# Optimization experiments

Measured on AMD Instinct MI355X. Metric: run time of the kernel, lower is better.

Reference implementation:

```python
import jax, jax.numpy as jnp
import numpy as np

NPAT, NCON, E, H, L = 50000, 20000, 800000, 128, 2
DP, DC = 64, 128
N = NPAT + NCON  # homogeneous node count


def setup_inputs() -> dict:
    key = jax.random.key(0)
    k = jax.random.split(key, 12)
    s = 0.05
    return {
        "x_patient": jax.random.normal(k[0], (NPAT, DP), jnp.float32),
        "x_concept": jax.random.normal(k[1], (NCON, DC), jnp.float32),
        "W_p": jax.random.normal(k[2], (DP, H), jnp.float32) * s,
        "b_p": jnp.zeros((H,), jnp.float32),
        "W_c": jax.random.normal(k[3], (DC, H), jnp.float32) * s,
        "b_c": jnp.zeros((H,), jnp.float32),
        "W_root": jax.random.normal(k[4], (L, H, H), jnp.float32) * s,
        "b_root": jnp.zeros((L, H), jnp.float32),
        "W_rel": jax.random.normal(k[5], (L, 2, H, H), jnp.float32) * s,
        "src_pc": jax.random.randint(k[6], (E,), 0, NPAT),
        "dst_pc": jax.random.randint(k[7], (E,), 0, NCON),
        "src_cp": jax.random.randint(k[8], (E,), 0, NCON),
        "dst_cp": jax.random.randint(k[9], (E,), 0, NPAT),
    }


def reference(x_patient, x_concept, W_p, b_p, W_c, b_c, W_root, b_root, W_rel,
              src_pc, dst_pc, src_cp, dst_cp):
    # per-node-type linear projection, then concat into homogeneous graph
    # (patient offset 0, concept offset NPAT)
    x = jnp.concatenate([x_patient @ W_p + b_p, x_concept @ W_c + b_c], axis=0)  # [N, H]
    rel_edges = [(src_pc, dst_pc + NPAT), (src_cp + NPAT, dst_cp)]
    ones = jnp.ones((E,), jnp.float32)
    # per-relation in-degree for mean aggregation (zero-deg nodes -> 0 output)
    counts = [jnp.maximum(jax.ops.segment_sum(ones, d, num_segments=N), 1.0)[:, None]
              for _, d in rel_edges]
    for l in range(L):
        out = x @ W_root[l] + b_root[l]  # root transform + bias
        for r, (src, dst) in enumerate(rel_edges):
            msg = x[src] @ W_rel[l, r]  # [E, H] gather + relation transform
            out = out + jax.ops.segment_sum(msg, dst, num_segments=N) / counts[r]
        x = jax.nn.relu(out)
    return x  # [N, H]; rows [0:NPAT] are patient embeddings, rest concepts
```

## Files before the change

kernel.cpp:

```cpp
#include <hip/hip_runtime.h>
#include <hip/hip_bf16.h>

#define NPAT 50000
#define NCON 20000
#define NN   70000
#define EE   800000
#define H    128

#define NCON_AL  20032
#define SEGN     (NCON_AL + NPAT)
#define NBUCK    1095
#define RELSPLIT_B 313
#define BUCKCAP  5120
#define SUBS     16
#define SUBCAP   (BUCKCAP / SUBS)
#define BPE      4096
#define NBB      ((2 * EE + BPE - 1) / BPE)
#define CAP      4096

typedef __attribute__((ext_vector_type(8))) short bf16x8;
typedef __attribute__((ext_vector_type(4))) float f32x4;

__device__ inline unsigned short f2bf(float f) {
    unsigned u = __float_as_uint(f);
    unsigned r = (u + 0x7FFFu + ((u >> 16) & 1u)) >> 16;
    return (unsigned short)r;
}
__device__ inline float bf2f_lo(unsigned v) { return __uint_as_float(v << 16); }
__device__ inline float bf2f_hi(unsigned v) { return __uint_as_float(v & 0xFFFF0000u); }

__global__ void init_gcur_kernel(int* __restrict__ gcur) {
    int j = blockIdx.x * 256 + threadIdx.x;
    if (j < NBUCK * SUBS) gcur[j] = (j >> 4) * BUCKCAP + (j & (SUBS - 1)) * SUBCAP;
}

__global__ __launch_bounds__(512) void binpack_kernel(
        const int* __restrict__ dst_pc, const int* __restrict__ src_pc,
        const int* __restrict__ dst_cp, const int* __restrict__ src_cp,
        int* __restrict__ gcur, unsigned* __restrict__ pairs) {
    __shared__ unsigned sval[BPE];
    __shared__ unsigned short sbkt[BPE];
    __shared__ int cnt[NBUCK];
    __shared__ int delta[NBUCK];
    __shared__ int partial[512];
    int t = threadIdx.x, blk = blockIdx.x;
    int base = blk * BPE;
    int n = min(BPE, 2 * EE - base);

    for (int i = t; i < NBUCK; i += 512) cnt[i] = 0;
    __syncthreads();

    unsigned pay[8];
    int bkt[8];
#pragma unroll
    for (int q = 0; q < 8; q++) {
        int li = q * 512 + t;
        bkt[q] = -1;
        if (li < n) {
            int i = base + li;
            int seg, src;
            if (i < EE) { seg = dst_pc[i];                src = src_pc[i]; }
            else        { seg = NCON_AL + dst_cp[i - EE]; src = src_cp[i - EE]; }
            int b = seg >> 6;
            pay[q] = (unsigned)src | ((unsigned)(seg & 63) << 16);
            bkt[q] = b;
            atomicAdd(&cnt[b], 1);
        }
    }
    __syncthreads();

    const int PER = (NBUCK + 511) / 512;
    int beg = t * PER;
    int s = 0;
#pragma unroll
    for (int k = 0; k < PER; k++) { int i = beg + k; if (i < NBUCK) s += cnt[i]; }
    partial[t] = s;
    __syncthreads();
    for (int o = 1; o < 512; o <<= 1) {
        int v = (t >= o) ? partial[t - o] : 0;
        __syncthreads();
        partial[t] += v;
        __syncthreads();
    }
    int run = partial[t] - s;
    int sub = blk & (SUBS - 1);
    int prefk[PER];
#pragma unroll
    for (int k = 0; k < PER; k++) {
        int i = beg + k;
        if (i < NBUCK) {
            prefk[k] = run;
            int c = cnt[i];
            if (c > 0) {
                int gb = atomicAdd(&gcur[i * SUBS + sub], c);
                delta[i] = gb - run;
            }
            run += c;
        }
    }
    __syncthreads();
#pragma unroll
    for (int k = 0; k < PER; k++) { int i = beg + k; if (i < NBUCK) cnt[i] = prefk[k]; }
    __syncthreads();

#pragma unroll
    for (int q = 0; q < 8; q++) {
        if (bkt[q] >= 0) {
            int b = bkt[q];
            int pos = atomicAdd(&cnt[b], 1);
            sval[pos] = pay[q];
            sbkt[pos] = (unsigned short)b;
        }
    }
    __syncthreads();
    for (int i = t; i < n; i += 512)
        pairs[delta[sbkt[i]] + i] = sval[i];
}

__global__ __launch_bounds__(512) void build_ssrc_kernel(
        const unsigned* __restrict__ pairs, const int* __restrict__ gcur,
        int* __restrict__ soffg) {
    __shared__ int cnt64[64];
    __shared__ int soff[65];
    __shared__ int scur[64];
    __shared__ unsigned short ssrc[CAP];
    int t = threadIdx.x, b = blockIdx.x;
    if (t < 64) cnt64[t] = 0;
    __syncthreads();
    for (int s = 0; s < SUBS; s++) {
        int rbase = b * BUCKCAP + s * SUBCAP;
        int rcnt = gcur[b * SUBS + s] - rbase;
        for (int i = t; i < rcnt; i += 512)
            atomicAdd(&cnt64[pairs[rbase + i] >> 16], 1);
    }
    __syncthreads();
    if (t < 64) {
        int v = cnt64[t];
        int s = v;
#pragma unroll
        for (int o = 1; o < 64; o <<= 1) {
            int u = __shfl_up(s, o);
            if (t >= o) s += u;
        }
        soff[t + 1] = s;
        if (t == 0) soff[0] = 0;
        scur[t] = s - v;
    }
    __syncthreads();
    for (int s = 0; s < SUBS; s++) {
        int rbase = b * BUCKCAP + s * SUBCAP;
        int rcnt = gcur[b * SUBS + s] - rbase;
        for (int i = t; i < rcnt; i += 512) {
            unsigned p = pairs[rbase + i];
            int pos = atomicAdd(&scur[p >> 16], 1);
            ssrc[pos] = (unsigned short)(p & 0xFFFF);
        }
    }
    __syncthreads();
    if (t < 65) soffg[b * 65 + t] = soff[t];
    int tot = soff[64];
    unsigned* sg = (unsigned*)(((unsigned short*)pairs) + (size_t)b * BUCKCAP * 2);
    const unsigned* sl = (const unsigned*)ssrc;
    for (int i = t; i < ((tot + 1) >> 1); i += 512) sg[i] = sl[i];
}

#define ACC8(a0, a1, v) \
    a0.x += bf2f_lo((v).x); a0.y += bf2f_hi((v).x); \
    a0.z += bf2f_lo((v).y); a0.w += bf2f_hi((v).y); \
    a1.x += bf2f_lo((v).z); a1.y += bf2f_hi((v).z); \
    a1.z += bf2f_lo((v).w); a1.w += bf2f_hi((v).w);

__global__ __launch_bounds__(512) void gather_kernel(
        const unsigned short* __restrict__ xbf,
        const unsigned short* __restrict__ ssrcg,
        const int* __restrict__ soffg,
        unsigned short* __restrict__ aggn) {
    __shared__ int soff[65];
    __shared__ unsigned short ssrc[CAP];
    int t = threadIdx.x, b = blockIdx.x;
    if (t < 65) soff[t] = soffg[b * 65 + t];
    __syncthreads();
    int tot = soff[64];
    const unsigned* sg = (const unsigned*)(ssrcg + (size_t)b * BUCKCAP * 2);
    unsigned* sl = (unsigned*)ssrc;
    for (int i = t; i < ((tot + 1) >> 1); i += 512) sl[i] = sg[i];
    __syncthreads();
    int wv = t >> 6, lane = t & 63;
    int g = lane >> 4;
    int q = lane & 15;
    int rowbase = (b < RELSPLIT_B) ? 0 : NPAT;
    int seglim  = (b < RELSPLIT_B) ? NCON : SEGN;
    const uint4* xw4 = (const uint4*)xbf;
    for (int i = 0; i < 8; i++) {
        int d = wv * 8 + i;
        int seg = b * 64 + d;
        if (seg >= seglim) continue;
        int beg = soff[d], end = soff[d + 1];
        float4 aA0 = {0.f, 0.f, 0.f, 0.f}, aA1 = {0.f, 0.f, 0.f, 0.f};
        float4 aB0 = {0.f, 0.f, 0.f, 0.f}, aB1 = {0.f, 0.f, 0.f, 0.f};
        int j = beg;
        for (; j + 7 < end; j += 8) {
            int sA = ssrc[j + g];
            int sB = ssrc[j + 4 + g];
            uint4 vA = xw4[(size_t)(rowbase + sA) * 16 + q];
            uint4 vB = xw4[(size_t)(rowbase + sB) * 16 + q];
            ACC8(aA0, aA1, vA);
            ACC8(aB0, aB1, vB);
        }
        for (; j < end; j += 4) {
            if (g < end - j) {
                int s0 = ssrc[j + g];
                uint4 v = xw4[(size_t)(rowbase + s0) * 16 + q];
                ACC8(aA0, aA1, v);
            }
        }
        aA0.x += aB0.x; aA0.y += aB0.y; aA0.z += aB0.z; aA0.w += aB0.w;
        aA1.x += aB1.x; aA1.y += aB1.y; aA1.z += aB1.z; aA1.w += aB1.w;
        float r0 = aA0.x, r1 = aA0.y, r2 = aA0.z, r3 = aA0.w;
        float r4 = aA1.x, r5 = aA1.y, r6 = aA1.z, r7 = aA1.w;
        r0 += __shfl_xor(r0, 16); r1 += __shfl_xor(r1, 16);
        r2 += __shfl_xor(r2, 16); r3 += __shfl_xor(r3, 16);
        r4 += __shfl_xor(r4, 16); r5 += __shfl_xor(r5, 16);
        r6 += __shfl_xor(r6, 16); r7 += __shfl_xor(r7, 16);
        r0 += __shfl_xor(r0, 32); r1 += __shfl_xor(r1, 32);
        r2 += __shfl_xor(r2, 32); r3 += __shfl_xor(r3, 32);
        r4 += __shfl_xor(r4, 32); r5 += __shfl_xor(r5, 32);
        r6 += __shfl_xor(r6, 32); r7 += __shfl_xor(r7, 32);
        if (g == 0) {
            float inv = 1.0f / (float)max(end - beg, 1);
            uint4 o;
            o.x = (unsigned)f2bf(r0 * inv) | ((unsigned)f2bf(r1 * inv) << 16);
            o.y = (unsigned)f2bf(r2 * inv) | ((unsigned)f2bf(r3 * inv) << 16);
            o.z = (unsigned)f2bf(r4 * inv) | ((unsigned)f2bf(r5 * inv) << 16);
            o.w = (unsigned)f2bf(r6 * inv) | ((unsigned)f2bf(r7 * inv) << 16);
            *(uint4*)&aggn[(size_t)seg * H + 8 * q] = o;
        }
    }
}

#define BM 128
#define BK 8

struct GemmJob {
    const float* A1;
    const float* B1;
    const float* bias; unsigned short* Cbf;
    int lda1, K1, M;
};

__global__ void gemm_dual_kernel(GemmJob j0, GemmJob j1, int nb0) {
    __shared__ float sA[BK][BM];
    __shared__ float sB[BK][H];
    bool first = (int)blockIdx.x < nb0;
    GemmJob j = first ? j0 : j1;
    int bm = (first ? blockIdx.x : blockIdx.x - nb0) * BM;
    int tid = threadIdx.x;
    int am = tid >> 1;
    int ak = (tid & 1) * 4;
    int bk = tid >> 5;
    int bn = (tid & 31) * 4;
    int ty = tid >> 4;
    int tx = tid & 15;
    float acc[8][8] = {};
    for (int k0 = 0; k0 < j.K1; k0 += BK) {
        int gm = bm + am; if (gm >= j.M) gm = j.M - 1;
        float4 av = *(const float4*)&j.A1[(size_t)gm * j.lda1 + k0 + ak];
        float4 bv = *(const float4*)&j.B1[(size_t)(k0 + bk) * H + bn];
        __syncthreads();
        sA[ak + 0][am] = av.x; sA[ak + 1][am] = av.y;
        sA[ak + 2][am] = av.z; sA[ak + 3][am] = av.w;
        *(float4*)&sB[bk][bn] = bv;
        __syncthreads();
#pragma unroll
        for (int k = 0; k < BK; k++) {
            float a[8], bb[8];
            *(float4*)&a[0] = *(const float4*)&sA[k][ty * 8];
            *(float4*)&a[4] = *(const float4*)&sA[k][ty * 8 + 4];
            *(float4*)&bb[0] = *(const float4*)&sB[k][tx * 4];
            *(float4*)&bb[4] = *(const float4*)&sB[k][64 + tx * 4];
#pragma unroll
            for (int i = 0; i < 8; i++)
#pragma unroll
                for (int jj = 0; jj < 8; jj++)
                    acc[i][jj] += a[i] * bb[jj];
        }
    }
    float bcol[8];
    *(float4*)&bcol[0] = *(const float4*)&j.bias[tx * 4];
    *(float4*)&bcol[4] = *(const float4*)&j.bias[64 + tx * 4];
#pragma unroll
    for (int i = 0; i < 8; i++) {
        int gr = bm + ty * 8 + i;
        if (gr < j.M) {
#pragma unroll
            for (int q = 0; q < 8; q++) {
                float v = acc[i][q] + bcol[q];
                int gc = (q < 4) ? (tx * 4 + q) : (64 + tx * 4 + q - 4);
                j.Cbf[(size_t)gr * H + gc] = f2bf(v);
            }
        }
    }
}

struct MJob {
    const unsigned short* A1;
    const unsigned short* A2;
    const float* B1;
    const float* B2;
    const float* bias;
    float* C;
    unsigned short* Cbf;
    int M;
};

__global__ __launch_bounds__(256) void gemm_mfma_kernel(MJob j0, MJob j1, int nb0) {
    __shared__ unsigned short sA[128][40];
    __shared__ unsigned short sBT[128][40];
    bool first = (int)blockIdx.x < nb0;
    MJob J = first ? j0 : j1;
    int bm = (first ? (int)blockIdx.x : (int)blockIdx.x - nb0) * 128;
    int tid = threadIdx.x;
    int wv = tid >> 6, lane = tid & 63;
    int wr = wv >> 1, wc = wv & 1;
    int m16 = lane & 15, kg = lane >> 4;

    f32x4 acc[4][4];
#pragma unroll
    for (int a = 0; a < 4; a++)
#pragma unroll
        for (int c = 0; c < 4; c++) acc[a][c] = (f32x4){0.f, 0.f, 0.f, 0.f};

    int ar = tid >> 1, ah = tid & 1;
    int gmA = bm + ar; if (gmA >= J.M) gmA = J.M - 1;
    int bn = tid & 127, bk0 = tid >> 7;

#pragma unroll
    for (int kt = 0; kt < 8; kt++) {
        int k0 = kt * 32;
        const unsigned short* asrc = (k0 < 128)
            ? (J.A1 + (size_t)gmA * H + k0)
            : (J.A2 + (size_t)gmA * H + (k0 - 128));
        const uint4* a4 = (const uint4*)(asrc + ah * 16);
        uint4 av0 = a4[0], av1 = a4[1];
        const float* bsrc = (k0 < 128) ? (J.B1 + (size_t)k0 * H)
                                       : (J.B2 + (size_t)(k0 - 128) * H);
        float bvals[16];
#pragma unroll
        for (int kk = 0; kk < 16; kk++) bvals[kk] = bsrc[(size_t)(2 * kk + bk0) * H + bn];
        __syncthreads();
        { uint4* d4 = (uint4*)&sA[ar][ah * 16]; d4[0] = av0; d4[1] = av1; }
#pragma unroll
        for (int kk = 0; kk < 16; kk++) sBT[bn][2 * kk + bk0] = f2bf(bvals[kk]);
        __syncthreads();
        bf16x8 af[4], bfg[4];
#pragma unroll
        for (int mt = 0; mt < 4; mt++)
            af[mt] = *(bf16x8*)&sA[wr * 64 + mt * 16 + m16][kg * 8];
#pragma unroll
        for (int nt = 0; nt < 4; nt++)
            bfg[nt] = *(bf16x8*)&sBT[wc * 64 + nt * 16 + m16][kg * 8];
#pragma unroll
        for (int mt = 0; mt < 4; mt++)
#pragma unroll
            for (int nt = 0; nt < 4; nt++)
                acc[mt][nt] = __builtin_amdgcn_mfma_f32_16x16x32_bf16(
                    af[mt], bfg[nt], acc[mt][nt], 0, 0, 0);
    }
    float bv[4];
#pragma unroll
    for (int nt = 0; nt < 4; nt++) bv[nt] = J.bias[wc * 64 + nt * 16 + m16];
#pragma unroll
    for (int mt = 0; mt < 4; mt++) {
        int gr0 = bm + wr * 64 + mt * 16 + kg * 4;
#pragma unroll
        for (int r = 0; r < 4; r++) {
            int gr = gr0 + r;
            if (gr < J.M) {
#pragma unroll
                for (int nt = 0; nt < 4; nt++) {
                    int gc = wc * 64 + nt * 16 + m16;
                    float v = fmaxf(acc[mt][nt][r] + bv[nt], 0.f);
                    if (J.C)   J.C[(size_t)gr * H + gc] = v;
                    if (J.Cbf) J.Cbf[(size_t)gr * H + gc] = f2bf(v);
                }
            }
        }
    }
}


extern "C" void kernel_launch(void* const* d_in, const int* in_sizes, int n_in,
                              void* d_out, int out_size, void* d_ws, size_t ws_size,
                              hipStream_t stream) {
    const float* x_patient = (const float*)d_in[0];
    const float* x_concept = (const float*)d_in[1];
    const float* W_p       = (const float*)d_in[2];
    const float* b_p       = (const float*)d_in[3];
    const float* W_c       = (const float*)d_in[4];
    const float* b_c       = (const float*)d_in[5];
    const float* W_root    = (const float*)d_in[6];
    const float* b_root    = (const float*)d_in[7];
    const float* W_rel     = (const float*)d_in[8];
    const int*   src_pc    = (const int*)d_in[9];
    const int*   dst_pc    = (const int*)d_in[10];
    const int*   src_cp    = (const int*)d_in[11];
    const int*   dst_cp    = (const int*)d_in[12];
    float* out = (float*)d_out;

    char* w = (char*)d_ws;
    unsigned short* xbf  = (unsigned short*)w; w += (size_t)NN * H * 2;
    unsigned short* aggn = (unsigned short*)w; w += (size_t)SEGN * H * 2;
    int* gcur = (int*)w;            w += (size_t)NBUCK * SUBS * 4;
    unsigned* pairs = (unsigned*)w; w += (size_t)NBUCK * BUCKCAP * 4;
    int* soffg = (int*)w;           w += (size_t)NBUCK * 65 * 4;

    init_gcur_kernel<<<(NBUCK * SUBS + 255) / 256, 256, 0, stream>>>(gcur);
    binpack_kernel<<<NBB, 512, 0, stream>>>(dst_pc, src_pc, dst_cp, src_cp, gcur, pairs);
    build_ssrc_kernel<<<NBUCK, 512, 0, stream>>>(pairs, gcur, soffg);
    const unsigned short* ssrcg = (const unsigned short*)pairs;

    const int PB = (NPAT + BM - 1) / BM;
    const int CB = (NCON + BM - 1) / BM;

    {
        GemmJob jp = { x_patient, W_p, b_p, xbf, 64, 64, NPAT };
        GemmJob jc = { x_concept, W_c, b_c, xbf + (size_t)NPAT * H, 128, 128, NCON };
        gemm_dual_kernel<<<PB + CB, 256, 0, stream>>>(jp, jc, PB);
    }

    for (int l = 0; l < 2; l++) {
        gather_kernel<<<NBUCK, 512, 0, stream>>>(xbf, ssrcg, soffg, aggn);
        const float* Wroot_l = W_root + (size_t)l * H * H;
        const float* Wrel_l0 = W_rel + (size_t)(l * 2 + 0) * H * H;
        const float* Wrel_l1 = W_rel + (size_t)(l * 2 + 1) * H * H;
        const float* br = b_root + (size_t)l * H;
        float* cp = (l == 1) ? out : nullptr;
        float* cc = (l == 1) ? out + (size_t)NPAT * H : nullptr;
        unsigned short* bp = (l == 0) ? xbf : nullptr;
        unsigned short* bc = (l == 0) ? xbf + (size_t)NPAT * H : nullptr;
        MJob jp = { xbf, aggn + (size_t)NCON_AL * H, Wroot_l, Wrel_l1, br,
                    cp, bp, NPAT };
        MJob jc = { xbf + (size_t)NPAT * H, aggn, Wroot_l, Wrel_l0, br,
                    cc, bc, NCON };
        gemm_mfma_kernel<<<PB + CB, 256, 0, stream>>>(jp, jc, PB);
    }
}
```

Baseline: 314.2 us.

## Partition gather edges by source-row range to improve cache locality

Edges in each destination bucket are sub-sorted into 8 source-index ranges, and the gather kernel walks one range at a time across all 64 destinations. Per-destination partial sums live in an LDS accumulator and are normalized at the end. The aim is to keep the source rows touched by a block at any moment inside a smaller address window, so L2 and MALL hit more often. In exchange it adds more offset bookkeeping, about 33KB of extra LDS per block (which may lower occupancy), and more short, partially empty inner loops.

```diff
diff --git a/kernel.cpp b/kernel.cpp
--- a/kernel.cpp
+++ b/kernel.cpp
@@ -17,6 +17,8 @@
 #define BPE      4096
 #define NBB      ((2 * EE + BPE - 1) / BPE)
 #define CAP      4096
+#define RMAX     8
+#define NOFF     (64 * RMAX + 1)
 
 typedef __attribute__((ext_vector_type(8))) short bf16x8;
 typedef __attribute__((ext_vector_type(4))) float f32x4;
@@ -120,45 +122,57 @@
 __global__ __launch_bounds__(512) void build_ssrc_kernel(
         const unsigned* __restrict__ pairs, const int* __restrict__ gcur,
         int* __restrict__ soffg) {
-    __shared__ int cnt64[64];
-    __shared__ int soff[65];
-    __shared__ int scur[64];
+    __shared__ int cnt[512];
+    __shared__ int soff[NOFF];
+    __shared__ int scur[512];
+    __shared__ int wtot[8];
     __shared__ unsigned short ssrc[CAP];
     int t = threadIdx.x, b = blockIdx.x;
-    if (t < 64) cnt64[t] = 0;
-    __syncthreads();
-    for (int s = 0; s < SUBS; s++) {
-        int rbase = b * BUCKCAP + s * SUBCAP;
-        int rcnt = gcur[b * SUBS + s] - rbase;
-        for (int i = t; i < rcnt; i += 512)
-            atomicAdd(&cnt64[pairs[rbase + i] >> 16], 1);
-    }
-    __syncthreads();
-    if (t < 64) {
-        int v = cnt64[t];
-        int s = v;
-#pragma unroll
-        for (int o = 1; o < 64; o <<= 1) {
-            int u = __shfl_up(s, o);
-            if (t >= o) s += u;
-        }
-        soff[t + 1] = s;
-        if (t == 0) soff[0] = 0;
-        scur[t] = s - v;
-    }
+    int sh = (b < RELSPLIT_B) ? 13 : 12;
+    cnt[t] = 0;
     __syncthreads();
     for (int s = 0; s < SUBS; s++) {
         int rbase = b * BUCKCAP + s * SUBCAP;
         int rcnt = gcur[b * SUBS + s] - rbase;
         for (int i = t; i < rcnt; i += 512) {
             unsigned p = pairs[rbase + i];
-            int pos = atomicAdd(&scur[p >> 16], 1);
+            atomicAdd(&cnt[(p >> 16) * RMAX + ((p & 0xFFFF) >> sh)], 1);
+        }
+    }
+    __syncthreads();
+    int wv = t >> 6, lane = t & 63;
+    int v = cnt[t];
+    int s = v;
+#pragma unroll
+    for (int o = 1; o < 64; o <<= 1) {
+        int u = __shfl_up(s, o);
+        if (lane >= o) s += u;
+    }
+    if (lane == 63) wtot[wv] = s;
+    __syncthreads();
+    if (t == 0) {
+        int run = 0;
+#pragma unroll
+        for (int k = 0; k < 8; k++) { int tmp = wtot[k]; wtot[k] = run; run += tmp; }
+    }
+    __syncthreads();
+    int incl = s + wtot[wv];
+    soff[t + 1] = incl;
+    if (t == 0) soff[0] = 0;
+    scur[t] = incl - v;
+    __syncthreads();
+    for (int s2 = 0; s2 < SUBS; s2++) {
+        int rbase = b * BUCKCAP + s2 * SUBCAP;
+        int rcnt = gcur[b * SUBS + s2] - rbase;
+        for (int i = t; i < rcnt; i += 512) {
+            unsigned p = pairs[rbase + i];
+            int pos = atomicAdd(&scur[(p >> 16) * RMAX + ((p & 0xFFFF) >> sh)], 1);
             ssrc[pos] = (unsigned short)(p & 0xFFFF);
         }
     }
     __syncthreads();
-    if (t < 65) soffg[b * 65 + t] = soff[t];
-    int tot = soff[64];
+    for (int i = t; i < NOFF; i += 512) soffg[b * NOFF + i] = soff[i];
+    int tot = soff[NOFF - 1];
     unsigned* sg = (unsigned*)(((unsigned short*)pairs) + (size_t)b * BUCKCAP * 2);
     const unsigned* sl = (const unsigned*)ssrc;
     for (int i = t; i < ((tot + 1) >> 1); i += 512) sg[i] = sl[i];
@@ -170,17 +184,26 @@
     a1.x += bf2f_lo((v).z); a1.y += bf2f_hi((v).z); \
     a1.z += bf2f_lo((v).w); a1.w += bf2f_hi((v).w);
 
+#define ACCPITCH 132
+
 __global__ __launch_bounds__(512) void gather_kernel(
         const unsigned short* __restrict__ xbf,
         const unsigned short* __restrict__ ssrcg,
         const int* __restrict__ soffg,
         unsigned short* __restrict__ aggn) {
-    __shared__ int soff[65];
+    __shared__ int soff[NOFF];
     __shared__ unsigned short ssrc[CAP];
+    __shared__ float accL[64 * ACCPITCH];
     int t = threadIdx.x, b = blockIdx.x;
-    if (t < 65) soff[t] = soffg[b * 65 + t];
-    __syncthreads();
-    int tot = soff[64];
+    for (int i = t; i < NOFF; i += 512) soff[i] = soffg[b * NOFF + i];
+    {
+        float4 z = {0.f, 0.f, 0.f, 0.f};
+        float* rp = &accL[(t >> 3) * ACCPITCH + (t & 7) * 16];
+        *(float4*)&rp[0] = z; *(float4*)&rp[4] = z;
+        *(float4*)&rp[8] = z; *(float4*)&rp[12] = z;
+    }
+    __syncthreads();
+    int tot = soff[NOFF - 1];
     const unsigned* sg = (const unsigned*)(ssrcg + (size_t)b * BUCKCAP * 2);
     unsigned* sl = (unsigned*)ssrc;
     for (int i = t; i < ((tot + 1) >> 1); i += 512) sl[i] = sg[i];
@@ -191,50 +214,66 @@
     int rowbase = (b < RELSPLIT_B) ? 0 : NPAT;
     int seglim  = (b < RELSPLIT_B) ? NCON : SEGN;
     const uint4* xw4 = (const uint4*)xbf;
+    for (int r = 0; r < RMAX; r++) {
+        for (int i = 0; i < 8; i++) {
+            int d = wv * 8 + i;
+            int seg = b * 64 + d;
+            if (seg >= seglim) continue;
+            int beg = soff[d * RMAX + r], end = soff[d * RMAX + r + 1];
+            if (beg == end) continue;
+            float4 aA0 = {0.f, 0.f, 0.f, 0.f}, aA1 = {0.f, 0.f, 0.f, 0.f};
+            float4 aB0 = {0.f, 0.f, 0.f, 0.f}, aB1 = {0.f, 0.f, 0.f, 0.f};
+            int j = beg;
+            for (; j + 7 < end; j += 8) {
+                int sA = ssrc[j + g];
+                int sB = ssrc[j + 4 + g];
+                uint4 vA = xw4[(size_t)(rowbase + sA) * 16 + q];
+                uint4 vB = xw4[(size_t)(rowbase + sB) * 16 + q];
+                ACC8(aA0, aA1, vA);
+                ACC8(aB0, aB1, vB);
+            }
+            for (; j < end; j += 4) {
+                if (g < end - j) {
+                    int s0 = ssrc[j + g];
+                    uint4 v = xw4[(size_t)(rowbase + s0) * 16 + q];
+                    ACC8(aA0, aA1, v);
+                }
+            }
+            aA0.x += aB0.x; aA0.y += aB0.y; aA0.z += aB0.z; aA0.w += aB0.w;
+            aA1.x += aB1.x; aA1.y += aB1.y; aA1.z += aB1.z; aA1.w += aB1.w;
+            float r0 = aA0.x, r1 = aA0.y, r2 = aA0.z, r3 = aA0.w;
+            float r4 = aA1.x, r5 = aA1.y, r6 = aA1.z, r7 = aA1.w;
+            r0 += __shfl_xor(r0, 16); r1 += __shfl_xor(r1, 16);
+            r2 += __shfl_xor(r2, 16); r3 += __shfl_xor(r3, 16);
+            r4 += __shfl_xor(r4, 16); r5 += __shfl_xor(r5, 16);
+            r6 += __shfl_xor(r6, 16); r7 += __shfl_xor(r7, 16);
+            r0 += __shfl_xor(r0, 32); r1 += __shfl_xor(r1, 32);
+            r2 += __shfl_xor(r2, 32); r3 += __shfl_xor(r3, 32);
+            r4 += __shfl_xor(r4, 32); r5 += __shfl_xor(r5, 32);
+            r6 += __shfl_xor(r6, 32); r7 += __shfl_xor(r7, 32);
+            if (g == 0) {
+                float* ap = &accL[d * ACCPITCH + 8 * q];
+                float4 p0 = *(float4*)&ap[0], p1 = *(float4*)&ap[4];
+                p0.x += r0; p0.y += r1; p0.z += r2; p0.w += r3;
+                p1.x += r4; p1.y += r5; p1.z += r6; p1.w += r7;
+                *(float4*)&ap[0] = p0; *(float4*)&ap[4] = p1;
+            }
+        }
+    }
     for (int i = 0; i < 8; i++) {
         int d = wv * 8 + i;
         int seg = b * 64 + d;
-        if (seg >= seglim) continue;
-        int beg = soff[d], end = soff[d + 1];
-        float4 aA0 = {0.f, 0.f, 0.f, 0.f}, aA1 = {0.f, 0.f, 0.f, 0.f};
-        float4 aB0 = {0.f, 0.f, 0.f, 0.f}, aB1 = {0.f, 0.f, 0.f, 0.f};
-        int j = beg;
-        for (; j + 7 < end; j += 8) {
-            int sA = ssrc[j + g];
-            int sB = ssrc[j + 4 + g];
-            uint4 vA = xw4[(size_t)(rowbase + sA) * 16 + q];
-            uint4 vB = xw4[(size_t)(rowbase + sB) * 16 + q];
-            ACC8(aA0, aA1, vA);
-            ACC8(aB0, aB1, vB);
-        }
-        for (; j < end; j += 4) {
-            if (g < end - j) {
-                int s0 = ssrc[j + g];
-                uint4 v = xw4[(size_t)(rowbase + s0) * 16 + q];
-                ACC8(aA0, aA1, v);
-            }
-        }
-        aA0.x += aB0.x; aA0.y += aB0.y; aA0.z += aB0.z; aA0.w += aB0.w;
-        aA1.x += aB1.x; aA1.y += aB1.y; aA1.z += aB1.z; aA1.w += aB1.w;
-        float r0 = aA0.x, r1 = aA0.y, r2 = aA0.z, r3 = aA0.w;
-        float r4 = aA1.x, r5 = aA1.y, r6 = aA1.z, r7 = aA1.w;
-        r0 += __shfl_xor(r0, 16); r1 += __shfl_xor(r1, 16);
-        r2 += __shfl_xor(r2, 16); r3 += __shfl_xor(r3, 16);
-        r4 += __shfl_xor(r4, 16); r5 += __shfl_xor(r5, 16);
-        r6 += __shfl_xor(r6, 16); r7 += __shfl_xor(r7, 16);
-        r0 += __shfl_xor(r0, 32); r1 += __shfl_xor(r1, 32);
-        r2 += __shfl_xor(r2, 32); r3 += __shfl_xor(r3, 32);
-        r4 += __shfl_xor(r4, 32); r5 += __shfl_xor(r5, 32);
-        r6 += __shfl_xor(r6, 32); r7 += __shfl_xor(r7, 32);
-        if (g == 0) {
-            float inv = 1.0f / (float)max(end - beg, 1);
-            uint4 o;
-            o.x = (unsigned)f2bf(r0 * inv) | ((unsigned)f2bf(r1 * inv) << 16);
-            o.y = (unsigned)f2bf(r2 * inv) | ((unsigned)f2bf(r3 * inv) << 16);
-            o.z = (unsigned)f2bf(r4 * inv) | ((unsigned)f2bf(r5 * inv) << 16);
-            o.w = (unsigned)f2bf(r6 * inv) | ((unsigned)f2bf(r7 * inv) << 16);
-            *(uint4*)&aggn[(size_t)seg * H + 8 * q] = o;
-        }
+        if (seg >= seglim || g != 0) continue;
+        int deg = soff[(d + 1) * RMAX] - soff[d * RMAX];
+        float inv = 1.0f / (float)max(deg, 1);
+        const float* ap = &accL[d * ACCPITCH + 8 * q];
+        float4 p0 = *(const float4*)&ap[0], p1 = *(const float4*)&ap[4];
+        uint4 o;
+        o.x = (unsigned)f2bf(p0.x * inv) | ((unsigned)f2bf(p0.y * inv) << 16);
+        o.y = (unsigned)f2bf(p0.z * inv) | ((unsigned)f2bf(p0.w * inv) << 16);
+        o.z = (unsigned)f2bf(p1.x * inv) | ((unsigned)f2bf(p1.y * inv) << 16);
+        o.w = (unsigned)f2bf(p1.z * inv) | ((unsigned)f2bf(p1.w * inv) << 16);
+        *(uint4*)&aggn[(size_t)seg * H + 8 * q] = o;
     }
 }
 
@@ -412,7 +451,7 @@
     unsigned short* aggn = (unsigned short*)w; w += (size_t)SEGN * H * 2;
     int* gcur = (int*)w;            w += (size_t)NBUCK * SUBS * 4;
     unsigned* pairs = (unsigned*)w; w += (size_t)NBUCK * BUCKCAP * 4;
-    int* soffg = (int*)w;           w += (size_t)NBUCK * 65 * 4;
+    int* soffg = (int*)w;           w += (size_t)NBUCK * NOFF * 4;
 
     init_gcur_kernel<<<(NBUCK * SUBS + 255) / 256, 256, 0, stream>>>(gcur);
     binpack_kernel<<<NBB, 512, 0, stream>>>(dst_pc, src_pc, dst_cp, src_cp, gcur, pairs);
```

After: 451.7 us. 1.44x slower.

## Fuse neighbor gather-mean into per-layer MFMA GEMM kernel via LDS aggregation tile

Applied to the files above, without the earlier changes.

Each RGCN layer now runs as one kernel. A block first gathers and mean-aggregates the neighbor rows for its 128-row tile (two 64-segment buckets) into an LDS bf16 tile, then runs the root and relation GEMM, taking the relation A operand straight from LDS. This removes the global aggn round-trip and one launch per layer. Because layer 1 reads layer 0's output while other blocks gather, a second bf16 buffer is added. The binpack prefix scan also switches from an LDS Hillis-Steele loop to wave shuffles plus a small cross-wave scan, cutting the number of barriers.

```diff
diff --git a/kernel.cpp b/kernel.cpp
--- a/kernel.cpp
+++ b/kernel.cpp
@@ -18,6 +18,11 @@
 #define NBB      ((2 * EE + BPE - 1) / BPE)
 #define CAP      4096
 
+#define BM 128
+#define BK 8
+#define PB_T 391
+#define CB_T 157
+
 typedef __attribute__((ext_vector_type(8))) short bf16x8;
 typedef __attribute__((ext_vector_type(4))) float f32x4;
 
@@ -42,7 +47,7 @@
     __shared__ unsigned short sbkt[BPE];
     __shared__ int cnt[NBUCK];
     __shared__ int delta[NBUCK];
-    __shared__ int partial[512];
+    __shared__ int wtot[8];
     int t = threadIdx.x, blk = blockIdx.x;
     int base = blk * BPE;
     int n = min(BPE, 2 * EE - base);
@@ -74,15 +79,23 @@
     int s = 0;
 #pragma unroll
     for (int k = 0; k < PER; k++) { int i = beg + k; if (i < NBUCK) s += cnt[i]; }
-    partial[t] = s;
-    __syncthreads();
-    for (int o = 1; o < 512; o <<= 1) {
-        int v = (t >= o) ? partial[t - o] : 0;
-        __syncthreads();
-        partial[t] += v;
-        __syncthreads();
-    }
-    int run = partial[t] - s;
+    int lane = t & 63, w8 = t >> 6;
+    int incl = s;
+#pragma unroll
+    for (int o = 1; o < 64; o <<= 1) {
+        int u = __shfl_up(incl, o);
+        if (lane >= o) incl += u;
+    }
+    if (lane == 63) wtot[w8] = incl;
+    __syncthreads();
+    if (t == 0) {
+        int r0 = 0;
+#pragma unroll
+        for (int k = 0; k < 8; k++) { int tmp = wtot[k]; wtot[k] = r0; r0 += tmp; }
+    }
+    __syncthreads();
+    int run = incl - s + wtot[w8];
+
     int sub = blk & (SUBS - 1);
     int prefk[PER];
 #pragma unroll
@@ -163,83 +176,6 @@
     const unsigned* sl = (const unsigned*)ssrc;
     for (int i = t; i < ((tot + 1) >> 1); i += 512) sg[i] = sl[i];
 }
-
-#define ACC8(a0, a1, v) \
-    a0.x += bf2f_lo((v).x); a0.y += bf2f_hi((v).x); \
-    a0.z += bf2f_lo((v).y); a0.w += bf2f_hi((v).y); \
-    a1.x += bf2f_lo((v).z); a1.y += bf2f_hi((v).z); \
-    a1.z += bf2f_lo((v).w); a1.w += bf2f_hi((v).w);
-
-__global__ __launch_bounds__(512) void gather_kernel(
-        const unsigned short* __restrict__ xbf,
-        const unsigned short* __restrict__ ssrcg,
-        const int* __restrict__ soffg,
-        unsigned short* __restrict__ aggn) {
-    __shared__ int soff[65];
-    __shared__ unsigned short ssrc[CAP];
-    int t = threadIdx.x, b = blockIdx.x;
-    if (t < 65) soff[t] = soffg[b * 65 + t];
-    __syncthreads();
-    int tot = soff[64];
-    const unsigned* sg = (const unsigned*)(ssrcg + (size_t)b * BUCKCAP * 2);
-    unsigned* sl = (unsigned*)ssrc;
-    for (int i = t; i < ((tot + 1) >> 1); i += 512) sl[i] = sg[i];
-    __syncthreads();
-    int wv = t >> 6, lane = t & 63;
-    int g = lane >> 4;
-    int q = lane & 15;
-    int rowbase = (b < RELSPLIT_B) ? 0 : NPAT;
-    int seglim  = (b < RELSPLIT_B) ? NCON : SEGN;
-    const uint4* xw4 = (const uint4*)xbf;
-    for (int i = 0; i < 8; i++) {
-        int d = wv * 8 + i;
-        int seg = b * 64 + d;
-        if (seg >= seglim) continue;
-        int beg = soff[d], end = soff[d + 1];
-        float4 aA0 = {0.f, 0.f, 0.f, 0.f}, aA1 = {0.f, 0.f, 0.f, 0.f};
-        float4 aB0 = {0.f, 0.f, 0.f, 0.f}, aB1 = {0.f, 0.f, 0.f, 0.f};
-        int j = beg;
-        for (; j + 7 < end; j += 8) {
-            int sA = ssrc[j + g];
-            int sB = ssrc[j + 4 + g];
-            uint4 vA = xw4[(size_t)(rowbase + sA) * 16 + q];
-            uint4 vB = xw4[(size_t)(rowbase + sB) * 16 + q];
-            ACC8(aA0, aA1, vA);
-            ACC8(aB0, aB1, vB);
-        }
-        for (; j < end; j += 4) {
-            if (g < end - j) {
-                int s0 = ssrc[j + g];
-                uint4 v = xw4[(size_t)(rowbase + s0) * 16 + q];
-                ACC8(aA0, aA1, v);
-            }
-        }
-        aA0.x += aB0.x; aA0.y += aB0.y; aA0.z += aB0.z; aA0.w += aB0.w;
-        aA1.x += aB1.x; aA1.y += aB1.y; aA1.z += aB1.z; aA1.w += aB1.w;
-        float r0 = aA0.x, r1 = aA0.y, r2 = aA0.z, r3 = aA0.w;
-        float r4 = aA1.x, r5 = aA1.y, r6 = aA1.z, r7 = aA1.w;
-        r0 += __shfl_xor(r0, 16); r1 += __shfl_xor(r1, 16);
-        r2 += __shfl_xor(r2, 16); r3 += __shfl_xor(r3, 16);
-        r4 += __shfl_xor(r4, 16); r5 += __shfl_xor(r5, 16);
-        r6 += __shfl_xor(r6, 16); r7 += __shfl_xor(r7, 16);
-        r0 += __shfl_xor(r0, 32); r1 += __shfl_xor(r1, 32);
-        r2 += __shfl_xor(r2, 32); r3 += __shfl_xor(r3, 32);
-        r4 += __shfl_xor(r4, 32); r5 += __shfl_xor(r5, 32);
-        r6 += __shfl_xor(r6, 32); r7 += __shfl_xor(r7, 32);
-        if (g == 0) {
-            float inv = 1.0f / (float)max(end - beg, 1);
-            uint4 o;
-            o.x = (unsigned)f2bf(r0 * inv) | ((unsigned)f2bf(r1 * inv) << 16);
-            o.y = (unsigned)f2bf(r2 * inv) | ((unsigned)f2bf(r3 * inv) << 16);
-            o.z = (unsigned)f2bf(r4 * inv) | ((unsigned)f2bf(r5 * inv) << 16);
-            o.w = (unsigned)f2bf(r6 * inv) | ((unsigned)f2bf(r7 * inv) << 16);
-            *(uint4*)&aggn[(size_t)seg * H + 8 * q] = o;
-        }
-    }
-}
-
-#define BM 128
-#define BK 8
 
 struct GemmJob {
     const float* A1;
@@ -302,65 +238,146 @@
     }
 }
 
-struct MJob {
-    const unsigned short* A1;
-    const unsigned short* A2;
-    const float* B1;
-    const float* B2;
-    const float* bias;
-    float* C;
-    unsigned short* Cbf;
-    int M;
-};
-
-__global__ __launch_bounds__(256) void gemm_mfma_kernel(MJob j0, MJob j1, int nb0) {
-    __shared__ unsigned short sA[128][40];
-    __shared__ unsigned short sBT[128][40];
-    bool first = (int)blockIdx.x < nb0;
-    MJob J = first ? j0 : j1;
-    int bm = (first ? (int)blockIdx.x : (int)blockIdx.x - nb0) * 128;
-    int tid = threadIdx.x;
-    int wv = tid >> 6, lane = tid & 63;
+#define ACC8(a0, a1, v) \
+    a0.x += bf2f_lo((v).x); a0.y += bf2f_hi((v).x); \
+    a0.z += bf2f_lo((v).y); a0.w += bf2f_hi((v).y); \
+    a1.x += bf2f_lo((v).z); a1.y += bf2f_hi((v).z); \
+    a1.z += bf2f_lo((v).w); a1.w += bf2f_hi((v).w);
+
+__global__ __launch_bounds__(512) void gmf_kernel(
+        const unsigned short* __restrict__ X,
+        const unsigned short* __restrict__ ssrcg,
+        const int* __restrict__ soffg,
+        const float* __restrict__ Broot,
+        const float* __restrict__ Brel0,
+        const float* __restrict__ Brel1,
+        const float* __restrict__ bias,
+        float* __restrict__ Cf,
+        unsigned short* __restrict__ Cbf) {
+    __shared__ union {
+        struct { int soff[2][65]; unsigned short ssrc[2][CAP]; } g;
+        struct { unsigned short sA[128][40]; unsigned short sBT[128][40]; } m;
+    } sm;
+    __shared__ unsigned short aggT[128][136];
+
+    int t = threadIdx.x;
+    int blk = blockIdx.x;
+    bool isC = blk < CB_T;
+    int tile = isC ? blk : blk - CB_T;
+    int bm = tile * 128;
+    int M = isC ? NCON : NPAT;
+    int b0 = isC ? 2 * tile : RELSPLIT_B + 2 * tile;
+    int rowbase = isC ? 0 : NPAT;
+    const unsigned short* A1 = X + (size_t)(isC ? NPAT : 0) * H;
+    const float* B2 = isC ? Brel0 : Brel1;
+    size_t crow0 = (size_t)(isC ? NPAT : 0) * H;
+
+    int nb = isC ? min(2, RELSPLIT_B - b0) : 2;
+#pragma unroll
+    for (int h = 0; h < 2; h++)
+        if (t < 65) sm.g.soff[h][t] = (h < nb) ? soffg[(b0 + h) * 65 + t] : 0;
+    __syncthreads();
+    for (int h = 0; h < nb; h++) {
+        int tot = sm.g.soff[h][64];
+        const unsigned* sg = (const unsigned*)(ssrcg + (size_t)(b0 + h) * BUCKCAP * 2);
+        unsigned* sl = (unsigned*)sm.g.ssrc[h];
+        for (int i = t; i < ((tot + 1) >> 1); i += 512) sl[i] = sg[i];
+    }
+    __syncthreads();
+    int wv = t >> 6, lane = t & 63;
+    int g = lane >> 4;
+    int q = lane & 15;
+    const uint4* xw4 = (const uint4*)X;
+    int seglim = isC ? NCON : SEGN;
+    for (int h = 0; h < nb; h++) {
+        int segbase = (b0 + h) * 64;
+        const unsigned short* ss = sm.g.ssrc[h];
+        for (int i = 0; i < 8; i++) {
+            int d = wv * 8 + i;
+            if (segbase + d >= seglim) continue;
+            int beg = sm.g.soff[h][d], end = sm.g.soff[h][d + 1];
+            float4 aA0 = {0.f, 0.f, 0.f, 0.f}, aA1 = {0.f, 0.f, 0.f, 0.f};
+            float4 aB0 = {0.f, 0.f, 0.f, 0.f}, aB1 = {0.f, 0.f, 0.f, 0.f};
+            int j = beg;
+            for (; j + 7 < end; j += 8) {
+                int sA_ = ss[j + g];
+                int sB_ = ss[j + 4 + g];
+                uint4 vA = xw4[(size_t)(rowbase + sA_) * 16 + q];
+                uint4 vB = xw4[(size_t)(rowbase + sB_) * 16 + q];
+                ACC8(aA0, aA1, vA);
+                ACC8(aB0, aB1, vB);
+            }
+            for (; j < end; j += 4) {
+                if (g < end - j) {
+                    int s0 = ss[j + g];
+                    uint4 v = xw4[(size_t)(rowbase + s0) * 16 + q];
+                    ACC8(aA0, aA1, v);
+                }
+            }
+            aA0.x += aB0.x; aA0.y += aB0.y; aA0.z += aB0.z; aA0.w += aB0.w;
+            aA1.x += aB1.x; aA1.y += aB1.y; aA1.z += aB1.z; aA1.w += aB1.w;
+            float r0 = aA0.x, r1 = aA0.y, r2 = aA0.z, r3 = aA0.w;
+            float r4 = aA1.x, r5 = aA1.y, r6 = aA1.z, r7 = aA1.w;
+            r0 += __shfl_xor(r0, 16); r1 += __shfl_xor(r1, 16);
+            r2 += __shfl_xor(r2, 16); r3 += __shfl_xor(r3, 16);
+            r4 += __shfl_xor(r4, 16); r5 += __shfl_xor(r5, 16);
+            r6 += __shfl_xor(r6, 16); r7 += __shfl_xor(r7, 16);
+            r0 += __shfl_xor(r0, 32); r1 += __shfl_xor(r1, 32);
+            r2 += __shfl_xor(r2, 32); r3 += __shfl_xor(r3, 32);
+            r4 += __shfl_xor(r4, 32); r5 += __shfl_xor(r5, 32);
+            r6 += __shfl_xor(r6, 32); r7 += __shfl_xor(r7, 32);
+            if (g == 0) {
+                float inv = 1.0f / (float)max(end - beg, 1);
+                uint4 o;
+                o.x = (unsigned)f2bf(r0 * inv) | ((unsigned)f2bf(r1 * inv) << 16);
+                o.y = (unsigned)f2bf(r2 * inv) | ((unsigned)f2bf(r3 * inv) << 16);
+                o.z = (unsigned)f2bf(r4 * inv) | ((unsigned)f2bf(r5 * inv) << 16);
+                o.w = (unsigned)f2bf(r6 * inv) | ((unsigned)f2bf(r7 * inv) << 16);
+                *(uint4*)&aggT[h * 64 + d][8 * q] = o;
+            }
+        }
+    }
+    __syncthreads();
+
     int wr = wv >> 1, wc = wv & 1;
     int m16 = lane & 15, kg = lane >> 4;
-
-    f32x4 acc[4][4];
-#pragma unroll
-    for (int a = 0; a < 4; a++)
-#pragma unroll
-        for (int c = 0; c < 4; c++) acc[a][c] = (f32x4){0.f, 0.f, 0.f, 0.f};
-
-    int ar = tid >> 1, ah = tid & 1;
-    int gmA = bm + ar; if (gmA >= J.M) gmA = J.M - 1;
-    int bn = tid & 127, bk0 = tid >> 7;
+    f32x4 acc[2][4];
+#pragma unroll
+    for (int mt = 0; mt < 2; mt++)
+#pragma unroll
+        for (int nt = 0; nt < 4; nt++) acc[mt][nt] = (f32x4){0.f, 0.f, 0.f, 0.f};
+
+    int ar = t >> 2, ah = t & 3;
+    int gmA = bm + ar; if (gmA >= M) gmA = M - 1;
+    int bn = t & 127, bq = t >> 7;
 
 #pragma unroll
     for (int kt = 0; kt < 8; kt++) {
         int k0 = kt * 32;
-        const unsigned short* asrc = (k0 < 128)
-            ? (J.A1 + (size_t)gmA * H + k0)
-            : (J.A2 + (size_t)gmA * H + (k0 - 128));
-        const uint4* a4 = (const uint4*)(asrc + ah * 16);
-        uint4 av0 = a4[0], av1 = a4[1];
-        const float* bsrc = (k0 < 128) ? (J.B1 + (size_t)k0 * H)
-                                       : (J.B2 + (size_t)(k0 - 128) * H);
-        float bvals[16];
-#pragma unroll
-        for (int kk = 0; kk < 16; kk++) bvals[kk] = bsrc[(size_t)(2 * kk + bk0) * H + bn];
+        uint4 av;
+        if (kt < 4) av = *(const uint4*)(A1 + (size_t)gmA * H + k0 + ah * 8);
+        const float* bsrc = (kt < 4) ? (Broot + (size_t)k0 * H)
+                                     : (B2 + (size_t)(k0 - 128) * H);
+        float bvals[8];
+#pragma unroll
+        for (int kk = 0; kk < 8; kk++) bvals[kk] = bsrc[(size_t)(bq * 8 + kk) * H + bn];
         __syncthreads();
-        { uint4* d4 = (uint4*)&sA[ar][ah * 16]; d4[0] = av0; d4[1] = av1; }
-#pragma unroll
-        for (int kk = 0; kk < 16; kk++) sBT[bn][2 * kk + bk0] = f2bf(bvals[kk]);
+        if (kt < 4) *(uint4*)&sm.m.sA[ar][ah * 8] = av;
+#pragma unroll
+        for (int kk = 0; kk < 8; kk++) sm.m.sBT[bn][bq * 8 + kk] = f2bf(bvals[kk]);
         __syncthreads();
-        bf16x8 af[4], bfg[4];
-#pragma unroll
-        for (int mt = 0; mt < 4; mt++)
-            af[mt] = *(bf16x8*)&sA[wr * 64 + mt * 16 + m16][kg * 8];
+        bf16x8 af[2], bfg[4];
+#pragma unroll
+        for (int mt = 0; mt < 2; mt++) {
+            int row = wr * 32 + mt * 16 + m16;
+            af[mt] = (kt < 4) ? *(bf16x8*)&sm.m.sA[row][kg * 8]
+                              : *(bf16x8*)&aggT[row][(k0 - 128) + kg * 8];
+        }
 #pragma unroll
         for (int nt = 0; nt < 4; nt++)
-            bfg[nt] = *(bf16x8*)&sBT[wc * 64 + nt * 16 + m16][kg * 8];
-#pragma unroll
-        for (int mt = 0; mt < 4; mt++)
+            bfg[nt] = *(bf16x8*)&sm.m.sBT[wc * 64 + nt * 16 + m16][kg * 8];
+#pragma unroll
+        for (int mt = 0; mt < 2; mt++)
 #pragma unroll
             for (int nt = 0; nt < 4; nt++)
                 acc[mt][nt] = __builtin_amdgcn_mfma_f32_16x16x32_bf16(
@@ -368,20 +385,20 @@
     }
     float bv[4];
 #pragma unroll
-    for (int nt = 0; nt < 4; nt++) bv[nt] = J.bias[wc * 64 + nt * 16 + m16];
-#pragma unroll
-    for (int mt = 0; mt < 4; mt++) {
-        int gr0 = bm + wr * 64 + mt * 16 + kg * 4;
+    for (int nt = 0; nt < 4; nt++) bv[nt] = bias[wc * 64 + nt * 16 + m16];
+#pragma unroll
+    for (int mt = 0; mt < 2; mt++) {
+        int gr0 = bm + wr * 32 + mt * 16 + kg * 4;
 #pragma unroll
         for (int r = 0; r < 4; r++) {
             int gr = gr0 + r;
-            if (gr < J.M) {
+            if (gr < M) {
 #pragma unroll
                 for (int nt = 0; nt < 4; nt++) {
                     int gc = wc * 64 + nt * 16 + m16;
                     float v = fmaxf(acc[mt][nt][r] + bv[nt], 0.f);
-                    if (J.C)   J.C[(size_t)gr * H + gc] = v;
-                    if (J.Cbf) J.Cbf[(size_t)gr * H + gc] = f2bf(v);
+                    if (Cf)  Cf[crow0 + (size_t)gr * H + gc] = v;
+                    if (Cbf) Cbf[crow0 + (size_t)gr * H + gc] = f2bf(v);
                 }
             }
         }
@@ -409,7 +426,7 @@
 
     char* w = (char*)d_ws;
     unsigned short* xbf  = (unsigned short*)w; w += (size_t)NN * H * 2;
-    unsigned short* aggn = (unsigned short*)w; w += (size_t)SEGN * H * 2;
+    unsigned short* xbf2 = (unsigned short*)w; w += (size_t)NN * H * 2;
     int* gcur = (int*)w;            w += (size_t)NBUCK * SUBS * 4;
     unsigned* pairs = (unsigned*)w; w += (size_t)NBUCK * BUCKCAP * 4;
     int* soffg = (int*)w;           w += (size_t)NBUCK * 65 * 4;
@@ -419,29 +436,20 @@
     build_ssrc_kernel<<<NBUCK, 512, 0, stream>>>(pairs, gcur, soffg);
     const unsigned short* ssrcg = (const unsigned short*)pairs;
 
-    const int PB = (NPAT + BM - 1) / BM;
-    const int CB = (NCON + BM - 1) / BM;
-
     {
         GemmJob jp = { x_patient, W_p, b_p, xbf, 64, 64, NPAT };
         GemmJob jc = { x_concept, W_c, b_c, xbf + (size_t)NPAT * H, 128, 128, NCON };
-        gemm_dual_kernel<<<PB + CB, 256, 0, stream>>>(jp, jc, PB);
+        gemm_dual_kernel<<<PB_T + CB_T, 256, 0, stream>>>(jp, jc, PB_T);
     }
 
     for (int l = 0; l < 2; l++) {
-        gather_kernel<<<NBUCK, 512, 0, stream>>>(xbf, ssrcg, soffg, aggn);
+        const unsigned short* X = l ? xbf2 : xbf;
         const float* Wroot_l = W_root + (size_t)l * H * H;
         const float* Wrel_l0 = W_rel + (size_t)(l * 2 + 0) * H * H;
         const float* Wrel_l1 = W_rel + (size_t)(l * 2 + 1) * H * H;
         const float* br = b_root + (size_t)l * H;
-        float* cp = (l == 1) ? out : nullptr;
-        float* cc = (l == 1) ? out + (size_t)NPAT * H : nullptr;
-        unsigned short* bp = (l == 0) ? xbf : nullptr;
-        unsigned short* bc = (l == 0) ? xbf + (size_t)NPAT * H : nullptr;
-        MJob jp = { xbf, aggn + (size_t)NCON_AL * H, Wroot_l, Wrel_l1, br,
-                    cp, bp, NPAT };
-        MJob jc = { xbf + (size_t)NPAT * H, aggn, Wroot_l, Wrel_l0, br,
-                    cc, bc, NCON };
-        gemm_mfma_kernel<<<PB + CB, 256, 0, stream>>>(jp, jc, PB);
-    }
-}
+        gmf_kernel<<<CB_T + PB_T, 512, 0, stream>>>(
+            X, ssrcg, soffg, Wroot_l, Wrel_l0, Wrel_l1, br,
+            l ? out : nullptr, l ? nullptr : xbf2);
+    }
+}
```

Result: slower. 335.7 us (+6.8%).

## Fuse input projection GEMM into binpack kernel and replace init with memset

Applied to the files above, without the earlier changes.

The fp32 input-projection GEMM is merged into the edge binpack kernel as extra blocks. Each 512-thread block runs two 128-row tiles in its two halves, so projection work overlaps with the edge bucketing and two kernel launches go away. The gcur init kernel becomes a memset: gcur now holds relative counts and the absolute bucket base is added at use. The block-wide prefix scan in binpack switches from a shared-memory Hillis-Steele loop to a wavefront shuffle scan. In exchange, the projection blocks now share a kernel with the much heavier binpack blocks, which may hurt occupancy.

```diff
diff --git a/kernel.cpp b/kernel.cpp
--- a/kernel.cpp
+++ b/kernel.cpp
@@ -18,6 +18,13 @@
 #define NBB      ((2 * EE + BPE - 1) / BPE)
 #define CAP      4096
 
+#define BM 128
+#define BK 8
+#define PB_T 391
+#define CB_T 157
+#define PPAIR_P 196
+#define PPAIR_C 79
+
 typedef __attribute__((ext_vector_type(8))) short bf16x8;
 typedef __attribute__((ext_vector_type(4))) float f32x4;
 
@@ -29,25 +36,97 @@
 __device__ inline float bf2f_lo(unsigned v) { return __uint_as_float(v << 16); }
 __device__ inline float bf2f_hi(unsigned v) { return __uint_as_float(v & 0xFFFF0000u); }
 
-__global__ void init_gcur_kernel(int* __restrict__ gcur) {
-    int j = blockIdx.x * 256 + threadIdx.x;
-    if (j < NBUCK * SUBS) gcur[j] = (j >> 4) * BUCKCAP + (j & (SUBS - 1)) * SUBCAP;
-}
-
-__global__ __launch_bounds__(512) void binpack_kernel(
+struct GemmJob {
+    const float* A1;
+    const float* B1;
+    const float* bias; unsigned short* Cbf;
+    int lda1, K1, M;
+};
+
+union BPSmem {
+    struct {
+        unsigned sval[BPE];
+        unsigned short sbkt[BPE];
+        int cnt[NBUCK];
+        int delta[NBUCK];
+        int wtot[8];
+    } b;
+    struct {
+        float sA[2][BK][BM];
+        float sB[2][BK][H];
+    } p;
+};
+
+__global__ __launch_bounds__(512) void binpack_proj_kernel(
         const int* __restrict__ dst_pc, const int* __restrict__ src_pc,
         const int* __restrict__ dst_cp, const int* __restrict__ src_cp,
-        int* __restrict__ gcur, unsigned* __restrict__ pairs) {
-    __shared__ unsigned sval[BPE];
-    __shared__ unsigned short sbkt[BPE];
-    __shared__ int cnt[NBUCK];
-    __shared__ int delta[NBUCK];
-    __shared__ int partial[512];
+        int* __restrict__ gcur, unsigned* __restrict__ pairs,
+        GemmJob j0, GemmJob j1) {
+    __shared__ BPSmem sm;
     int t = threadIdx.x, blk = blockIdx.x;
+
+    if (blk >= NBB) {
+        int half = t >> 8;
+        int tid = t & 255;
+        int pb = blk - NBB;
+        bool first = pb < PPAIR_P;
+        GemmJob j = first ? j0 : j1;
+        int ntiles = first ? PB_T : CB_T;
+        int tile = first ? pb * 2 + half : (pb - PPAIR_P) * 2 + half;
+        if (tile > ntiles) tile = ntiles;
+        int bm = tile * BM;
+        int am = tid >> 1;
+        int ak = (tid & 1) * 4;
+        int bk = tid >> 5;
+        int bn = (tid & 31) * 4;
+        int ty = tid >> 4;
+        int tx = tid & 15;
+        float acc[8][8] = {};
+        for (int k0 = 0; k0 < j.K1; k0 += BK) {
+            int gm = bm + am; if (gm >= j.M) gm = j.M - 1;
+            float4 av = *(const float4*)&j.A1[(size_t)gm * j.lda1 + k0 + ak];
+            float4 bv = *(const float4*)&j.B1[(size_t)(k0 + bk) * H + bn];
+            __syncthreads();
+            sm.p.sA[half][ak + 0][am] = av.x; sm.p.sA[half][ak + 1][am] = av.y;
+            sm.p.sA[half][ak + 2][am] = av.z; sm.p.sA[half][ak + 3][am] = av.w;
+            *(float4*)&sm.p.sB[half][bk][bn] = bv;
+            __syncthreads();
+#pragma unroll
+            for (int k = 0; k < BK; k++) {
+                float a[8], bb[8];
+                *(float4*)&a[0] = *(const float4*)&sm.p.sA[half][k][ty * 8];
+                *(float4*)&a[4] = *(const float4*)&sm.p.sA[half][k][ty * 8 + 4];
+                *(float4*)&bb[0] = *(const float4*)&sm.p.sB[half][k][tx * 4];
+                *(float4*)&bb[4] = *(const float4*)&sm.p.sB[half][k][64 + tx * 4];
+#pragma unroll
+                for (int i = 0; i < 8; i++)
+#pragma unroll
+                    for (int jj = 0; jj < 8; jj++)
+                        acc[i][jj] += a[i] * bb[jj];
+            }
+        }
+        float bcol[8];
+        *(float4*)&bcol[0] = *(const float4*)&j.bias[tx * 4];
+        *(float4*)&bcol[4] = *(const float4*)&j.bias[64 + tx * 4];
+#pragma unroll
+        for (int i = 0; i < 8; i++) {
+            int gr = bm + ty * 8 + i;
+            if (gr < j.M) {
+#pragma unroll
+                for (int q = 0; q < 8; q++) {
+                    float v = acc[i][q] + bcol[q];
+                    int gc = (q < 4) ? (tx * 4 + q) : (64 + tx * 4 + q - 4);
+                    j.Cbf[(size_t)gr * H + gc] = f2bf(v);
+                }
+            }
+        }
+        return;
+    }
+
     int base = blk * BPE;
     int n = min(BPE, 2 * EE - base);
 
-    for (int i = t; i < NBUCK; i += 512) cnt[i] = 0;
+    for (int i = t; i < NBUCK; i += 512) sm.b.cnt[i] = 0;
     __syncthreads();
 
     unsigned pay[8];
@@ -64,7 +143,7 @@
             int b = seg >> 6;
             pay[q] = (unsigned)src | ((unsigned)(seg & 63) << 16);
             bkt[q] = b;
-            atomicAdd(&cnt[b], 1);
+            atomicAdd(&sm.b.cnt[b], 1);
         }
     }
     __syncthreads();
@@ -73,16 +152,24 @@
     int beg = t * PER;
     int s = 0;
 #pragma unroll
-    for (int k = 0; k < PER; k++) { int i = beg + k; if (i < NBUCK) s += cnt[i]; }
-    partial[t] = s;
-    __syncthreads();
-    for (int o = 1; o < 512; o <<= 1) {
-        int v = (t >= o) ? partial[t - o] : 0;
-        __syncthreads();
-        partial[t] += v;
-        __syncthreads();
-    }
-    int run = partial[t] - s;
+    for (int k = 0; k < PER; k++) { int i = beg + k; if (i < NBUCK) s += sm.b.cnt[i]; }
+    int lane = t & 63, w8 = t >> 6;
+    int incl = s;
+#pragma unroll
+    for (int o = 1; o < 64; o <<= 1) {
+        int u = __shfl_up(incl, o);
+        if (lane >= o) incl += u;
+    }
+    if (lane == 63) sm.b.wtot[w8] = incl;
+    __syncthreads();
+    if (t == 0) {
+        int r0 = 0;
+#pragma unroll
+        for (int k = 0; k < 8; k++) { int tmp = sm.b.wtot[k]; sm.b.wtot[k] = r0; r0 += tmp; }
+    }
+    __syncthreads();
+    int run = incl - s + sm.b.wtot[w8];
+
     int sub = blk & (SUBS - 1);
     int prefk[PER];
 #pragma unroll
@@ -90,31 +177,31 @@
         int i = beg + k;
         if (i < NBUCK) {
             prefk[k] = run;
-            int c = cnt[i];
+            int c = sm.b.cnt[i];
             if (c > 0) {
                 int gb = atomicAdd(&gcur[i * SUBS + sub], c);
-                delta[i] = gb - run;
+                sm.b.delta[i] = (i * BUCKCAP + sub * SUBCAP + gb) - run;
             }
             run += c;
         }
     }
     __syncthreads();
 #pragma unroll
-    for (int k = 0; k < PER; k++) { int i = beg + k; if (i < NBUCK) cnt[i] = prefk[k]; }
+    for (int k = 0; k < PER; k++) { int i = beg + k; if (i < NBUCK) sm.b.cnt[i] = prefk[k]; }
     __syncthreads();
 
 #pragma unroll
     for (int q = 0; q < 8; q++) {
         if (bkt[q] >= 0) {
             int b = bkt[q];
-            int pos = atomicAdd(&cnt[b], 1);
-            sval[pos] = pay[q];
-            sbkt[pos] = (unsigned short)b;
+            int pos = atomicAdd(&sm.b.cnt[b], 1);
+            sm.b.sval[pos] = pay[q];
+            sm.b.sbkt[pos] = (unsigned short)b;
         }
     }
     __syncthreads();
     for (int i = t; i < n; i += 512)
-        pairs[delta[sbkt[i]] + i] = sval[i];
+        pairs[sm.b.delta[sm.b.sbkt[i]] + i] = sm.b.sval[i];
 }
 
 __global__ __launch_bounds__(512) void build_ssrc_kernel(
@@ -129,7 +216,7 @@
     __syncthreads();
     for (int s = 0; s < SUBS; s++) {
         int rbase = b * BUCKCAP + s * SUBCAP;
-        int rcnt = gcur[b * SUBS + s] - rbase;
+        int rcnt = gcur[b * SUBS + s];
         for (int i = t; i < rcnt; i += 512)
             atomicAdd(&cnt64[pairs[rbase + i] >> 16], 1);
     }
@@ -149,7 +236,7 @@
     __syncthreads();
     for (int s = 0; s < SUBS; s++) {
         int rbase = b * BUCKCAP + s * SUBCAP;
-        int rcnt = gcur[b * SUBS + s] - rbase;
+        int rcnt = gcur[b * SUBS + s];
         for (int i = t; i < rcnt; i += 512) {
             unsigned p = pairs[rbase + i];
             int pos = atomicAdd(&scur[p >> 16], 1);
@@ -238,70 +325,6 @@
     }
 }
 
-#define BM 128
-#define BK 8
-
-struct GemmJob {
-    const float* A1;
-    const float* B1;
-    const float* bias; unsigned short* Cbf;
-    int lda1, K1, M;
-};
-
-__global__ void gemm_dual_kernel(GemmJob j0, GemmJob j1, int nb0) {
-    __shared__ float sA[BK][BM];
-    __shared__ float sB[BK][H];
-    bool first = (int)blockIdx.x < nb0;
-    GemmJob j = first ? j0 : j1;
-    int bm = (first ? blockIdx.x : blockIdx.x - nb0) * BM;
-    int tid = threadIdx.x;
-    int am = tid >> 1;
-    int ak = (tid & 1) * 4;
-    int bk = tid >> 5;
-    int bn = (tid & 31) * 4;
-    int ty = tid >> 4;
-    int tx = tid & 15;
-    float acc[8][8] = {};
-    for (int k0 = 0; k0 < j.K1; k0 += BK) {
-        int gm = bm + am; if (gm >= j.M) gm = j.M - 1;
-        float4 av = *(const float4*)&j.A1[(size_t)gm * j.lda1 + k0 + ak];
-        float4 bv = *(const float4*)&j.B1[(size_t)(k0 + bk) * H + bn];
-        __syncthreads();
-        sA[ak + 0][am] = av.x; sA[ak + 1][am] = av.y;
-        sA[ak + 2][am] = av.z; sA[ak + 3][am] = av.w;
-        *(float4*)&sB[bk][bn] = bv;
-        __syncthreads();
-#pragma unroll
-        for (int k = 0; k < BK; k++) {
-            float a[8], bb[8];
-            *(float4*)&a[0] = *(const float4*)&sA[k][ty * 8];
-            *(float4*)&a[4] = *(const float4*)&sA[k][ty * 8 + 4];
-            *(float4*)&bb[0] = *(const float4*)&sB[k][tx * 4];
-            *(float4*)&bb[4] = *(const float4*)&sB[k][64 + tx * 4];
-#pragma unroll
-            for (int i = 0; i < 8; i++)
-#pragma unroll
-                for (int jj = 0; jj < 8; jj++)
-                    acc[i][jj] += a[i] * bb[jj];
-        }
-    }
-    float bcol[8];
-    *(float4*)&bcol[0] = *(const float4*)&j.bias[tx * 4];
-    *(float4*)&bcol[4] = *(const float4*)&j.bias[64 + tx * 4];
-#pragma unroll
-    for (int i = 0; i < 8; i++) {
-        int gr = bm + ty * 8 + i;
-        if (gr < j.M) {
-#pragma unroll
-            for (int q = 0; q < 8; q++) {
-                float v = acc[i][q] + bcol[q];
-                int gc = (q < 4) ? (tx * 4 + q) : (64 + tx * 4 + q - 4);
-                j.Cbf[(size_t)gr * H + gc] = f2bf(v);
-            }
-        }
-    }
-}
-
 struct MJob {
     const unsigned short* A1;
     const unsigned short* A2;
@@ -414,19 +437,16 @@
     unsigned* pairs = (unsigned*)w; w += (size_t)NBUCK * BUCKCAP * 4;
     int* soffg = (int*)w;           w += (size_t)NBUCK * 65 * 4;
 
-    init_gcur_kernel<<<(NBUCK * SUBS + 255) / 256, 256, 0, stream>>>(gcur);
-    binpack_kernel<<<NBB, 512, 0, stream>>>(dst_pc, src_pc, dst_cp, src_cp, gcur, pairs);
-    build_ssrc_kernel<<<NBUCK, 512, 0, stream>>>(pairs, gcur, soffg);
-    const unsigned short* ssrcg = (const unsigned short*)pairs;
-
-    const int PB = (NPAT + BM - 1) / BM;
-    const int CB = (NCON + BM - 1) / BM;
+    hipMemsetAsync(gcur, 0, (size_t)NBUCK * SUBS * 4, stream);
 
     {
         GemmJob jp = { x_patient, W_p, b_p, xbf, 64, 64, NPAT };
         GemmJob jc = { x_concept, W_c, b_c, xbf + (size_t)NPAT * H, 128, 128, NCON };
-        gemm_dual_kernel<<<PB + CB, 256, 0, stream>>>(jp, jc, PB);
-    }
+        binpack_proj_kernel<<<NBB + PPAIR_P + PPAIR_C, 512, 0, stream>>>(
+            dst_pc, src_pc, dst_cp, src_cp, gcur, pairs, jp, jc);
+    }
+    build_ssrc_kernel<<<NBUCK, 512, 0, stream>>>(pairs, gcur, soffg);
+    const unsigned short* ssrcg = (const unsigned short*)pairs;
 
     for (int l = 0; l < 2; l++) {
         gather_kernel<<<NBUCK, 512, 0, stream>>>(xbf, ssrcg, soffg, aggn);
@@ -442,6 +462,6 @@
                     cp, bp, NPAT };
         MJob jc = { xbf + (size_t)NPAT * H, aggn, Wroot_l, Wrel_l0, br,
                     cc, bc, NCON };
-        gemm_mfma_kernel<<<PB + CB, 256, 0, stream>>>(jp, jc, PB);
-    }
-}
+        gemm_mfma_kernel<<<PB_T + CB_T, 256, 0, stream>>>(jp, jc, PB_T);
+    }
+}
```

New measurement: 322.1 us. +2.5%, slower.
